# Optimization experiments

Hardware: AMD Instinct MI355X
Metric: run time of the kernel (lower is better)

The kernel has to match this reference:

```python
import jax, jax.numpy as jnp
import numpy as np

B, C, H, W = 4, 64, 128, 128
Q = 65536
OUT_SIZE = 256  # output image side -> cell = 2/OUT_SIZE
HIDDEN = 256
D_IN = C + 2 + 2  # feat + rel_coord + rel_cell


def setup_inputs() -> dict:
    key = jax.random.key(0)
    ks = jax.random.split(key, 8)
    feat = jax.random.normal(ks[0], (B, C, H, W), dtype=jnp.float32)
    coord = jax.random.uniform(ks[1], (B, Q, 2), dtype=jnp.float32, minval=-1.0, maxval=1.0)
    cell = jnp.full((B, Q, 2), 2.0 / OUT_SIZE, dtype=jnp.float32)

    def lin(k, din, dout):
        return jax.random.normal(k, (din, dout), dtype=jnp.float32) * (1.0 / np.sqrt(din))

    w0 = lin(ks[2], D_IN, HIDDEN)
    w1 = lin(ks[3], HIDDEN, HIDDEN)
    w2 = lin(ks[4], HIDDEN, HIDDEN)
    w3 = lin(ks[5], HIDDEN, HIDDEN)
    w4 = lin(ks[6], HIDDEN, 3)
    z = lambda d: jnp.zeros((d,), dtype=jnp.float32)
    return {"feat": feat, "coord": coord, "cell": cell,
            "w0": w0, "b0": z(HIDDEN), "w1": w1, "b1": z(HIDDEN),
            "w2": w2, "b2": z(HIDDEN), "w3": w3, "b3": z(HIDDEN),
            "w4": w4, "b4": z(3)}


def _liif(feat, coord, cell, ws, bs):
    b, c, h, w = feat.shape
    eps = 1e-6
    rx, ry = 1.0 / h, 1.0 / w  # 2/h/2, 2/w/2
    # local ensemble shifts, loop order vx outer, vy inner: (-1,-1),(-1,1),(1,-1),(1,1)
    shifts = jnp.array([[-rx, -ry], [-rx, ry], [rx, -ry], [rx, ry]], dtype=feat.dtype) + eps
    feat_flat = feat.reshape(b, c, h * w)
    cell_scale = jnp.array([h, w], dtype=feat.dtype)
    rel_cell = cell * cell_scale  # same for all branches

    def branch(shift):
        cshift = jnp.clip(coord + shift, -1.0 + eps, 1.0 - eps)
        # nearest grid_sample, align_corners=False: idx = floor((x+1)*size/2), clamped
        iy = jnp.clip(jnp.floor((cshift[..., 0] + 1.0) * (h * 0.5)), 0.0, h - 1.0).astype(jnp.int32)
        ix = jnp.clip(jnp.floor((cshift[..., 1] + 1.0) * (w * 0.5)), 0.0, w - 1.0).astype(jnp.int32)
        idx = iy * w + ix  # [B, Q]
        q_feat = jnp.take_along_axis(feat_flat, idx[:, None, :], axis=2)  # [B, C, Q]
        q_feat = q_feat.transpose(0, 2, 1)  # [B, Q, C]
        # feat_coord at the gathered pixel (make_coord values)
        qc0 = -1.0 + (2.0 * iy.astype(feat.dtype) + 1.0) / h
        qc1 = -1.0 + (2.0 * ix.astype(feat.dtype) + 1.0) / w
        rel0 = (coord[..., 0] - qc0) * h
        rel1 = (coord[..., 1] - qc1) * w
        inp = jnp.concatenate([q_feat, rel0[..., None], rel1[..., None], rel_cell], axis=-1)
        x = inp
        for wi, bi in zip(ws[:-1], bs[:-1]):
            x = jax.nn.relu(x @ wi + bi)
        pred = x @ ws[-1] + bs[-1]  # [B, Q, 3]
        area = jnp.abs(rel0 * rel1) + 1e-9  # [B, Q]
        return pred, area

    preds, areas = jax.vmap(branch)(shifts)  # [4,B,Q,3], [4,B,Q]
    tot = areas.sum(axis=0)
    # diagonal weight swap: 0<->3, 1<->2  == reverse
    wgt = areas[::-1] / tot
    return (preds * wgt[..., None]).sum(axis=0)  # [B, Q, 3]


def reference(feat, coord, cell, w0, b0, w1, b1, w2, b2, w3, b3, w4, b4):
    ws = [w0, w1, w2, w3, w4]
    bs = [b0, b1, b2, b3, b4]
    return _liif(feat, coord, cell, ws, bs)
```

## Files before the change

### kernel.cpp

```cpp
#include <hip/hip_runtime.h>
#include <cstdint>

typedef __bf16 bf16x8 __attribute__((ext_vector_type(8)));
typedef float f32x4 __attribute__((ext_vector_type(4)));
typedef unsigned int u32x4 __attribute__((ext_vector_type(4)));
typedef unsigned int u32x2 __attribute__((ext_vector_type(2)));
typedef unsigned short u16;
typedef unsigned int u32;

#define HH 128
#define WW 128
#define CC 64
#define QQ 65536
#define BB 4

#define RS 264

#define L0_OFF 0
#define L1_OFF 24576
#define L2_OFF 90112
#define L3_OFF 155648
#define W4_OFF 221184
#define FEATT_BYTE_OFF 524288u

__global__ void pack_weights(const float* __restrict__ w0,
                             const float* __restrict__ w1,
                             const float* __restrict__ w2,
                             const float* __restrict__ w3,
                             const float* __restrict__ w4,
                             u16* __restrict__ ws_us) {
    int bid = blockIdx.x;
    int lane = threadIdx.x;
    int tile, nk, off, Ksrc, Ncols, NT;
    const float* w;
    if (bid < 48)       { tile = bid;       nk = 3; off = L0_OFF; w = w0; Ksrc = 68;  Ncols = 256; NT = 16; }
    else if (bid < 176) { tile = bid - 48;  nk = 8; off = L1_OFF; w = w1; Ksrc = 256; Ncols = 256; NT = 16; }
    else if (bid < 304) { tile = bid - 176; nk = 8; off = L2_OFF; w = w2; Ksrc = 256; Ncols = 256; NT = 16; }
    else if (bid < 432) { tile = bid - 304; nk = 8; off = L3_OFF; w = w3; Ksrc = 256; Ncols = 256; NT = 16; }
    else                { tile = bid - 432; nk = 8; off = W4_OFF; w = w4; Ksrc = 256; Ncols = 3;   NT = 1;  }
    int kt = tile % nk;
    int nt = tile / nk;
    int n = nt * 16 + (lane & 15);
    int kbase = kt * 32 + (lane >> 4) * 8;
    unsigned int d[4];
    for (int i = 0; i < 4; ++i) {
        unsigned int lo, hi;
        {
            int k = kbase + 2 * i;
            float x = (k < Ksrc && n < Ncols) ? w[k * Ncols + n] : 0.0f;
            __bf16 hb = (__bf16)x;
            lo = (unsigned int)__builtin_bit_cast(u16, hb);
        }
        {
            int k = kbase + 2 * i + 1;
            float x = (k < Ksrc && n < Ncols) ? w[k * Ncols + n] : 0.0f;
            __bf16 hb = (__bf16)x;
            hi = (unsigned int)__builtin_bit_cast(u16, hb);
        }
        d[i] = lo | (hi << 16);
    }
    u32x4 pk = { d[0], d[1], d[2], d[3] };
    int dst = off + (kt * NT + nt) * 512 + lane * 8;
    *reinterpret_cast<u32x4*>(ws_us + dst) = pk;
}

__global__ void prep_featT(const float* __restrict__ feat, u16* __restrict__ featT) {
    __shared__ u16 tile[128 * 66];
    int bid = blockIdx.x;
    int b = bid >> 7, y = bid & 127;
    for (int idx = threadIdx.x; idx < CC * WW; idx += 256) {
        int c = idx >> 7, x = idx & 127;
        float v = feat[(((b * CC + c) * HH + y) * WW) + x];
        __bf16 hb = (__bf16)v;
        tile[x * 66 + c] = __builtin_bit_cast(u16, hb);
    }
    __syncthreads();
    for (int idx = threadIdx.x; idx < 2048; idx += 256) {
        int x = idx >> 4, c4 = (idx & 15) * 4;
        const u16* src = tile + x * 66 + c4;
        u32x2 d;
        d[0] = (unsigned int)src[0] | ((unsigned int)src[1] << 16);
        d[1] = (unsigned int)src[2] | ((unsigned int)src[3] << 16);
        *reinterpret_cast<u32x2*>(featT + ((b * HH + y) * WW + x) * CC + c4) = d;
    }
}

__device__ __forceinline__ void preload_w(u32x4 wpre[4], const u32x4* __restrict__ wbase,
                                          int voff) {
#pragma unroll
    for (int fi = 0; fi < 4; ++fi)
        wpre[fi] = wbase[voff + fi * 64];
}

template <int NK>
__device__ __forceinline__ void gemm_layer(u16* buf,
                                           const u32x4* __restrict__ wbase,
                                           const float* __restrict__ bias,
                                           int wave, int lane,
                                           const u32x4 wpre[4],
                                           u32x4 wnxt[4],
                                           const u32x4* __restrict__ wnb,
                                           int vnxt) {
    f32x4 acc[4][4] = {};
    const int l15 = lane & 15;
    const int qd = lane >> 4;
    const int voff = wave * 256 + lane;
    const u16* xb = buf + l15 * RS + qd * 8;
    u16* db = buf + l15 * RS + wave * 64 + qd * 4;

    u32x4 wq[2][4];
#pragma unroll
    for (int fi = 0; fi < 4; ++fi) wq[0][fi] = wpre[fi];

    bf16x8 xc[4];
#pragma unroll
    for (int st = 0; st < 4; ++st)
        xc[st] = __builtin_bit_cast(bf16x8,
            *reinterpret_cast<const u32x4*>(xb + st * 16 * RS));

#pragma unroll
    for (int kt = 0; kt < NK; ++kt) {
        if (kt + 1 < NK) {
            const u32x4* wn = wbase + (kt + 1) * 1024;
#pragma unroll
            for (int fi = 0; fi < 4; ++fi)
                wq[(kt + 1) & 1][fi] = wn[voff + fi * 64];
        }
#pragma unroll
        for (int st = 0; st < 4; ++st) {
#pragma unroll
            for (int fi = 0; fi < 4; ++fi)
                acc[fi][st] = __builtin_amdgcn_mfma_f32_16x16x32_bf16(
                    __builtin_bit_cast(bf16x8, wq[kt & 1][fi]), xc[st],
                    acc[fi][st], 0, 0, 0);
            if (kt + 1 < NK)
                xc[st] = __builtin_bit_cast(bf16x8,
                    *reinterpret_cast<const u32x4*>(xb + st * 16 * RS + (kt + 1) * 32));
        }
    }

#pragma unroll
    for (int fi = 0; fi < 4; ++fi) wnxt[fi] = wnb[vnxt + fi * 64];

    __syncthreads();

#pragma unroll
    for (int fi = 0; fi < 4; ++fi) {
        int fbase = (wave * 4 + fi) * 16 + qd * 4;
        f32x4 bv = *reinterpret_cast<const f32x4*>(bias + fbase);
#pragma unroll
        for (int st = 0; st < 4; ++st) {
            float v0 = fmaxf(acc[fi][st][0] + bv[0], 0.0f);
            float v1 = fmaxf(acc[fi][st][1] + bv[1], 0.0f);
            float v2 = fmaxf(acc[fi][st][2] + bv[2], 0.0f);
            float v3 = fmaxf(acc[fi][st][3] + bv[3], 0.0f);
            __bf16 h0 = (__bf16)v0, h1 = (__bf16)v1, h2 = (__bf16)v2, h3 = (__bf16)v3;
            u32x2 d;
            d[0] = (u32)__builtin_bit_cast(u16, h0) | ((u32)__builtin_bit_cast(u16, h1) << 16);
            d[1] = (u32)__builtin_bit_cast(u16, h2) | ((u32)__builtin_bit_cast(u16, h3) << 16);
            *reinterpret_cast<u32x2*>(db + st * 16 * RS + fi * 16) = d;
        }
    }
}

__global__ __launch_bounds__(256, 4) void liif_main(
    const float* __restrict__ coord, const float* __restrict__ cell,
    const float* __restrict__ b0, const float* __restrict__ b1,
    const float* __restrict__ b2, const float* __restrict__ b3,
    const float* __restrict__ b4,
    const u16* __restrict__ wpack, const u16* __restrict__ featT,
    float* __restrict__ out) {
    __shared__ u16 bufA[64 * RS];
    __shared__ float areasLDS[64];

    const int t = threadIdx.x;
    const int wave = t >> 6, lane = t & 63;
    const int row = t >> 2, p = t & 3;

    const int bq = blockIdx.x * 16 + (row >> 2);
    const int v = row & 3;
    const int b = bq >> 16;
    const float c0 = coord[bq * 2 + 0];
    const float c1 = coord[bq * 2 + 1];
    const float rc0 = cell[bq * 2 + 0] * 128.0f;
    const float rc1 = cell[bq * 2 + 1] * 128.0f;
    const float eps = 1e-6f;
    const float sx = ((v & 2) ? 0.0078125f : -0.0078125f) + eps;
    const float sy = ((v & 1) ? 0.0078125f : -0.0078125f) + eps;
    float cs0 = fminf(fmaxf(c0 + sx, -1.0f + eps), 1.0f - eps);
    float cs1 = fminf(fmaxf(c1 + sy, -1.0f + eps), 1.0f - eps);
    float fy = fminf(fmaxf(floorf((cs0 + 1.0f) * 64.0f), 0.0f), 127.0f);
    float fx = fminf(fmaxf(floorf((cs1 + 1.0f) * 64.0f), 0.0f), 127.0f);
    int iy = (int)fy, ix = (int)fx;
    float qc0 = -1.0f + (2.0f * fy + 1.0f) * 0.0078125f;
    float qc1 = -1.0f + (2.0f * fx + 1.0f) * 0.0078125f;
    float rel0 = (c0 - qc0) * 128.0f;
    float rel1 = (c1 - qc1) * 128.0f;
    float area = fabsf(rel0 * rel1) + 1e-9f;

    {
        const u16* fr = featT + (((b * HH + iy) * WW + ix) * CC) + p * 16;
        u32x4 f0 = *reinterpret_cast<const u32x4*>(fr);
        u32x4 f1 = *reinterpret_cast<const u32x4*>(fr + 8);
        u16* sb = bufA + row * RS;
        *reinterpret_cast<u32x4*>(sb + p * 16) = f0;
        *reinterpret_cast<u32x4*>(sb + p * 16 + 8) = f1;
        u32x4 e = { 0u, 0u, 0u, 0u };
        if (p == 0) {
            __bf16 h0 = (__bf16)rel0, h1 = (__bf16)rel1, h2 = (__bf16)rc0, h3 = (__bf16)rc1;
            e[0] = (u32)__builtin_bit_cast(u16, h0) | ((u32)__builtin_bit_cast(u16, h1) << 16);
            e[1] = (u32)__builtin_bit_cast(u16, h2) | ((u32)__builtin_bit_cast(u16, h3) << 16);
            areasLDS[row] = area;
        }
        *reinterpret_cast<u32x4*>(sb + 64 + p * 8) = e;
    }

    const u32x4* wp = reinterpret_cast<const u32x4*>(wpack);
    const u32x4* wp0 = wp + (L0_OFF / 8);
    const u32x4* wp1 = wp + (L1_OFF / 8);
    const u32x4* wp2 = wp + (L2_OFF / 8);
    const u32x4* wp3 = wp + (L3_OFF / 8);
    const u32x4* wp4 = wp + (W4_OFF / 8);
    const int voff = wave * 256 + lane;

    u32x4 wA[4], wB[4];
    preload_w(wA, wp0, voff);
    __syncthreads();
    gemm_layer<3>(bufA, wp0, b0, wave, lane, wA, wB, wp1, voff);
    __syncthreads();
    gemm_layer<8>(bufA, wp1, b1, wave, lane, wB, wA, wp2, voff);
    __syncthreads();
    gemm_layer<8>(bufA, wp2, b2, wave, lane, wA, wB, wp3, voff);
    __syncthreads();
    gemm_layer<8>(bufA, wp3, b3, wave, lane, wB, wA, wp4, lane);
    u32x4 w4hi[4];
#pragma unroll
    for (int kt = 0; kt < 4; ++kt) w4hi[kt] = wp4[(kt + 4) * 64 + lane];
    __syncthreads();

    const int l15 = lane & 15;
    const int qd = lane >> 4;
    const u16* xb = bufA + (wave * 16 + l15) * RS + qd * 8;
    f32x4 accf = {};
#pragma unroll
    for (int kt = 0; kt < 4; ++kt) {
        bf16x8 x = __builtin_bit_cast(bf16x8,
            *reinterpret_cast<const u32x4*>(xb + kt * 32));
        accf = __builtin_amdgcn_mfma_f32_16x16x32_bf16(
            __builtin_bit_cast(bf16x8, wA[kt]), x, accf, 0, 0, 0);
    }
#pragma unroll
    for (int kt = 4; kt < 8; ++kt) {
        bf16x8 x = __builtin_bit_cast(bf16x8,
            *reinterpret_cast<const u32x4*>(xb + kt * 32));
        accf = __builtin_amdgcn_mfma_f32_16x16x32_bf16(
            __builtin_bit_cast(bf16x8, w4hi[kt - 4]), x, accf, 0, 0, 0);
    }
    float a = areasLDS[wave * 16 + l15];
    float a1 = a + __shfl_xor(a, 1);
    float asum = a1 + __shfl_xor(a1, 2);
    float aopp = __shfl_xor(a, 3);
    float wgt = aopp / asum;
    float o0 = (accf[0] + b4[0]) * wgt;
    float o1 = (accf[1] + b4[1]) * wgt;
    float o2 = (accf[2] + b4[2]) * wgt;
    o0 += __shfl_xor(o0, 1); o0 += __shfl_xor(o0, 2);
    o1 += __shfl_xor(o1, 1); o1 += __shfl_xor(o1, 2);
    o2 += __shfl_xor(o2, 1); o2 += __shfl_xor(o2, 2);

    if (qd == 0 && (l15 & 3) == 0) {
        int obq = blockIdx.x * 16 + wave * 4 + (l15 >> 2);
        out[obq * 3 + 0] = o0;
        out[obq * 3 + 1] = o1;
        out[obq * 3 + 2] = o2;
    }
}

extern "C" void kernel_launch(void* const* d_in, const int* in_sizes, int n_in,
                              void* d_out, int out_size, void* d_ws, size_t ws_size,
                              hipStream_t stream) {
    const float* feat  = (const float*)d_in[0];
    const float* coord = (const float*)d_in[1];
    const float* cell  = (const float*)d_in[2];
    const float* w0 = (const float*)d_in[3];
    const float* b0 = (const float*)d_in[4];
    const float* w1 = (const float*)d_in[5];
    const float* b1 = (const float*)d_in[6];
    const float* w2 = (const float*)d_in[7];
    const float* b2 = (const float*)d_in[8];
    const float* w3 = (const float*)d_in[9];
    const float* b3 = (const float*)d_in[10];
    const float* w4 = (const float*)d_in[11];
    const float* b4 = (const float*)d_in[12];

    u16* ws_us = (u16*)d_ws;
    u16* featT = (u16*)((char*)d_ws + FEATT_BYTE_OFF);

    hipLaunchKernelGGL(pack_weights, dim3(440), dim3(64), 0, stream,
                       w0, w1, w2, w3, w4, ws_us);
    hipLaunchKernelGGL(prep_featT, dim3(BB * HH), dim3(256), 0, stream, feat, featT);
    hipLaunchKernelGGL(liif_main, dim3((BB * QQ) / 16), dim3(256), 0, stream,
                       coord, cell, b0, b1, b2, b3, b4, ws_us, featT,
                       (float*)d_out);
}
```

Before: 518.3 us.

## Split MLP feature columns across eight waves with ping-pong LDS activation buffers

Doubles the block to 512 threads, so each of eight waves computes 32 output features per layer instead of 64. Activations alternate between two LDS buffers, which removes the barrier inside each layer between the GEMM reads and the epilogue writes. Weight prefetch registers per wave are halved. In exchange, LDS use per block doubles, each wave reloads the full activation tile for half the MFMA work, and the final 3-output layer runs on only four of the eight waves.

Measured after the change: 537.0 us. 1.04x slower.

```diff
diff --git a/kernel.cpp b/kernel.cpp
--- a/kernel.cpp
+++ b/kernel.cpp
@@ -85,32 +85,26 @@
     }
 }
 
-__device__ __forceinline__ void preload_w(u32x4 wpre[4], const u32x4* __restrict__ wbase,
-                                          int voff) {
-#pragma unroll
-    for (int fi = 0; fi < 4; ++fi)
-        wpre[fi] = wbase[voff + fi * 64];
-}
-
 template <int NK>
-__device__ __forceinline__ void gemm_layer(u16* buf,
+__device__ __forceinline__ void gemm_layer(const u16* __restrict__ src,
+                                           u16* __restrict__ dst,
                                            const u32x4* __restrict__ wbase,
                                            const float* __restrict__ bias,
                                            int wave, int lane,
-                                           const u32x4 wpre[4],
-                                           u32x4 wnxt[4],
+                                           const u32x4 wpre[2],
+                                           u32x4 wnxt[2],
                                            const u32x4* __restrict__ wnb,
                                            int vnxt) {
-    f32x4 acc[4][4] = {};
+    f32x4 acc[2][4] = {};
     const int l15 = lane & 15;
     const int qd = lane >> 4;
-    const int voff = wave * 256 + lane;
-    const u16* xb = buf + l15 * RS + qd * 8;
-    u16* db = buf + l15 * RS + wave * 64 + qd * 4;
-
-    u32x4 wq[2][4];
-#pragma unroll
-    for (int fi = 0; fi < 4; ++fi) wq[0][fi] = wpre[fi];
+    const int voff = wave * 128 + lane;
+    const u16* xb = src + l15 * RS + qd * 8;
+    u16* db = dst + l15 * RS + wave * 32 + qd * 4;
+
+    u32x4 wq[2][2];
+    wq[0][0] = wpre[0];
+    wq[0][1] = wpre[1];
 
     bf16x8 xc[4];
 #pragma unroll
@@ -123,13 +117,13 @@
         if (kt + 1 < NK) {
             const u32x4* wn = wbase + (kt + 1) * 1024;
 #pragma unroll
-            for (int fi = 0; fi < 4; ++fi)
+            for (int fi = 0; fi < 2; ++fi)
                 wq[(kt + 1) & 1][fi] = wn[voff + fi * 64];
         }
 #pragma unroll
         for (int st = 0; st < 4; ++st) {
 #pragma unroll
-            for (int fi = 0; fi < 4; ++fi)
+            for (int fi = 0; fi < 2; ++fi)
                 acc[fi][st] = __builtin_amdgcn_mfma_f32_16x16x32_bf16(
                     __builtin_bit_cast(bf16x8, wq[kt & 1][fi]), xc[st],
                     acc[fi][st], 0, 0, 0);
@@ -140,13 +134,11 @@
     }
 
 #pragma unroll
-    for (int fi = 0; fi < 4; ++fi) wnxt[fi] = wnb[vnxt + fi * 64];
-
-    __syncthreads();
-
-#pragma unroll
-    for (int fi = 0; fi < 4; ++fi) {
-        int fbase = (wave * 4 + fi) * 16 + qd * 4;
+    for (int fi = 0; fi < 2; ++fi) wnxt[fi] = wnb[vnxt + fi * 64];
+
+#pragma unroll
+    for (int fi = 0; fi < 2; ++fi) {
+        int fbase = wave * 32 + fi * 16 + qd * 4;
         f32x4 bv = *reinterpret_cast<const f32x4*>(bias + fbase);
 #pragma unroll
         for (int st = 0; st < 4; ++st) {
@@ -163,7 +155,7 @@
     }
 }
 
-__global__ __launch_bounds__(256, 4) void liif_main(
+__global__ __launch_bounds__(512, 4) void liif_main(
     const float* __restrict__ coord, const float* __restrict__ cell,
     const float* __restrict__ b0, const float* __restrict__ b1,
     const float* __restrict__ b2, const float* __restrict__ b3,
@@ -171,11 +163,12 @@
     const u16* __restrict__ wpack, const u16* __restrict__ featT,
     float* __restrict__ out) {
     __shared__ u16 bufA[64 * RS];
+    __shared__ u16 bufB[64 * RS];
     __shared__ float areasLDS[64];
 
     const int t = threadIdx.x;
     const int wave = t >> 6, lane = t & 63;
-    const int row = t >> 2, p = t & 3;
+    const int row = t >> 3, p = t & 7;
 
     const int bq = blockIdx.x * 16 + (row >> 2);
     const int v = row & 3;
@@ -199,20 +192,20 @@
     float area = fabsf(rel0 * rel1) + 1e-9f;
 
     {
-        const u16* fr = featT + (((b * HH + iy) * WW + ix) * CC) + p * 16;
+        const u16* fr = featT + (((b * HH + iy) * WW + ix) * CC) + p * 8;
         u32x4 f0 = *reinterpret_cast<const u32x4*>(fr);
-        u32x4 f1 = *reinterpret_cast<const u32x4*>(fr + 8);
         u16* sb = bufA + row * RS;
-        *reinterpret_cast<u32x4*>(sb + p * 16) = f0;
-        *reinterpret_cast<u32x4*>(sb + p * 16 + 8) = f1;
-        u32x4 e = { 0u, 0u, 0u, 0u };
-        if (p == 0) {
-            __bf16 h0 = (__bf16)rel0, h1 = (__bf16)rel1, h2 = (__bf16)rc0, h3 = (__bf16)rc1;
-            e[0] = (u32)__builtin_bit_cast(u16, h0) | ((u32)__builtin_bit_cast(u16, h1) << 16);
-            e[1] = (u32)__builtin_bit_cast(u16, h2) | ((u32)__builtin_bit_cast(u16, h3) << 16);
-            areasLDS[row] = area;
-        }
-        *reinterpret_cast<u32x4*>(sb + 64 + p * 8) = e;
+        *reinterpret_cast<u32x4*>(sb + p * 8) = f0;
+        if (p < 4) {
+            u32x4 e = { 0u, 0u, 0u, 0u };
+            if (p == 0) {
+                __bf16 h0 = (__bf16)rel0, h1 = (__bf16)rel1, h2 = (__bf16)rc0, h3 = (__bf16)rc1;
+                e[0] = (u32)__builtin_bit_cast(u16, h0) | ((u32)__builtin_bit_cast(u16, h1) << 16);
+                e[1] = (u32)__builtin_bit_cast(u16, h2) | ((u32)__builtin_bit_cast(u16, h3) << 16);
+                areasLDS[row] = area;
+            }
+            *reinterpret_cast<u32x4*>(sb + 64 + p * 8) = e;
+        }
     }
 
     const u32x4* wp = reinterpret_cast<const u32x4*>(wpack);
@@ -221,58 +214,61 @@
     const u32x4* wp2 = wp + (L2_OFF / 8);
     const u32x4* wp3 = wp + (L3_OFF / 8);
     const u32x4* wp4 = wp + (W4_OFF / 8);
-    const int voff = wave * 256 + lane;
-
-    u32x4 wA[4], wB[4];
-    preload_w(wA, wp0, voff);
-    __syncthreads();
-    gemm_layer<3>(bufA, wp0, b0, wave, lane, wA, wB, wp1, voff);
-    __syncthreads();
-    gemm_layer<8>(bufA, wp1, b1, wave, lane, wB, wA, wp2, voff);
-    __syncthreads();
-    gemm_layer<8>(bufA, wp2, b2, wave, lane, wA, wB, wp3, voff);
-    __syncthreads();
-    gemm_layer<8>(bufA, wp3, b3, wave, lane, wB, wA, wp4, lane);
-    u32x4 w4hi[4];
-#pragma unroll
-    for (int kt = 0; kt < 4; ++kt) w4hi[kt] = wp4[(kt + 4) * 64 + lane];
-    __syncthreads();
-
-    const int l15 = lane & 15;
-    const int qd = lane >> 4;
-    const u16* xb = bufA + (wave * 16 + l15) * RS + qd * 8;
-    f32x4 accf = {};
-#pragma unroll
-    for (int kt = 0; kt < 4; ++kt) {
-        bf16x8 x = __builtin_bit_cast(bf16x8,
-            *reinterpret_cast<const u32x4*>(xb + kt * 32));
-        accf = __builtin_amdgcn_mfma_f32_16x16x32_bf16(
-            __builtin_bit_cast(bf16x8, wA[kt]), x, accf, 0, 0, 0);
-    }
-#pragma unroll
-    for (int kt = 4; kt < 8; ++kt) {
-        bf16x8 x = __builtin_bit_cast(bf16x8,
-            *reinterpret_cast<const u32x4*>(xb + kt * 32));
-        accf = __builtin_amdgcn_mfma_f32_16x16x32_bf16(
-            __builtin_bit_cast(bf16x8, w4hi[kt - 4]), x, accf, 0, 0, 0);
-    }
-    float a = areasLDS[wave * 16 + l15];
-    float a1 = a + __shfl_xor(a, 1);
-    float asum = a1 + __shfl_xor(a1, 2);
-    float aopp = __shfl_xor(a, 3);
-    float wgt = aopp / asum;
-    float o0 = (accf[0] + b4[0]) * wgt;
-    float o1 = (accf[1] + b4[1]) * wgt;
-    float o2 = (accf[2] + b4[2]) * wgt;
-    o0 += __shfl_xor(o0, 1); o0 += __shfl_xor(o0, 2);
-    o1 += __shfl_xor(o1, 1); o1 += __shfl_xor(o1, 2);
-    o2 += __shfl_xor(o2, 1); o2 += __shfl_xor(o2, 2);
-
-    if (qd == 0 && (l15 & 3) == 0) {
-        int obq = blockIdx.x * 16 + wave * 4 + (l15 >> 2);
-        out[obq * 3 + 0] = o0;
-        out[obq * 3 + 1] = o1;
-        out[obq * 3 + 2] = o2;
+    const int voff = wave * 128 + lane;
+
+    u32x4 wA[2], wB[2];
+    wA[0] = wp0[voff];
+    wA[1] = wp0[voff + 64];
+    __syncthreads();
+    gemm_layer<3>(bufA, bufB, wp0, b0, wave, lane, wA, wB, wp1, voff);
+    __syncthreads();
+    gemm_layer<8>(bufB, bufA, wp1, b1, wave, lane, wB, wA, wp2, voff);
+    __syncthreads();
+    gemm_layer<8>(bufA, bufB, wp2, b2, wave, lane, wA, wB, wp3, voff);
+    __syncthreads();
+    gemm_layer<8>(bufB, bufA, wp3, b3, wave, lane, wB, wA, wp4, lane);
+    u32x4 w4r[6];
+#pragma unroll
+    for (int i = 0; i < 6; ++i) w4r[i] = wp4[(i + 2) * 64 + lane];
+    __syncthreads();
+
+    if (wave < 4) {
+        const int l15 = lane & 15;
+        const int qd = lane >> 4;
+        const u16* xb = bufA + (wave * 16 + l15) * RS + qd * 8;
+        f32x4 accf = {};
+#pragma unroll
+        for (int kt = 0; kt < 2; ++kt) {
+            bf16x8 x = __builtin_bit_cast(bf16x8,
+                *reinterpret_cast<const u32x4*>(xb + kt * 32));
+            accf = __builtin_amdgcn_mfma_f32_16x16x32_bf16(
+                __builtin_bit_cast(bf16x8, wA[kt]), x, accf, 0, 0, 0);
+        }
+#pragma unroll
+        for (int kt = 2; kt < 8; ++kt) {
+            bf16x8 x = __builtin_bit_cast(bf16x8,
+                *reinterpret_cast<const u32x4*>(xb + kt * 32));
+            accf = __builtin_amdgcn_mfma_f32_16x16x32_bf16(
+                __builtin_bit_cast(bf16x8, w4r[kt - 2]), x, accf, 0, 0, 0);
+        }
+        float a = areasLDS[wave * 16 + l15];
+        float a1 = a + __shfl_xor(a, 1);
+        float asum = a1 + __shfl_xor(a1, 2);
+        float aopp = __shfl_xor(a, 3);
+        float wgt = aopp / asum;
+        float o0 = (accf[0] + b4[0]) * wgt;
+        float o1 = (accf[1] + b4[1]) * wgt;
+        float o2 = (accf[2] + b4[2]) * wgt;
+        o0 += __shfl_xor(o0, 1); o0 += __shfl_xor(o0, 2);
+        o1 += __shfl_xor(o1, 1); o1 += __shfl_xor(o1, 2);
+        o2 += __shfl_xor(o2, 1); o2 += __shfl_xor(o2, 2);
+
+        if (qd == 0 && (l15 & 3) == 0) {
+            int obq = blockIdx.x * 16 + wave * 4 + (l15 >> 2);
+            out[obq * 3 + 0] = o0;
+            out[obq * 3 + 1] = o1;
+            out[obq * 3 + 2] = o2;
+        }
     }
 }
 
@@ -299,7 +295,7 @@
     hipLaunchKernelGGL(pack_weights, dim3(440), dim3(64), 0, stream,
                        w0, w1, w2, w3, w4, ws_us);
     hipLaunchKernelGGL(prep_featT, dim3(BB * HH), dim3(256), 0, stream, feat, featT);
-    hipLaunchKernelGGL(liif_main, dim3((BB * QQ) / 16), dim3(256), 0, stream,
+    hipLaunchKernelGGL(liif_main, dim3((BB * QQ) / 16), dim3(512), 0, stream,
                        coord, cell, b0, b1, b2, b3, b4, ws_us, featT,
                        (float*)d_out);
 }
```
